# Optimization experiments

Hardware: AMD Instinct MI355X
Metric: run time of the kernel (lower is better)

Reference implementation:

```python
import jax, jax.numpy as jnp
import numpy as np

N, E, DIM, H = 50000, 800000, 64, 4

def setup_inputs() -> dict:
    key = jax.random.key(0)
    k0, k1, k2, k3, k4 = jax.random.split(key, 5)
    h_v = jax.random.normal(k0, (N, DIM), dtype=jnp.float32)
    src = jax.random.randint(k1, (E,), 0, N, dtype=jnp.int64)
    dst = jax.random.randint(k2, (E,), 0, N, dtype=jnp.int64)
    W_fc = jax.random.normal(k3, (DIM * H, DIM), dtype=jnp.float32) * 0.05
    b_fc = jnp.zeros((DIM * H,), dtype=jnp.float32)
    W_pi = jax.random.normal(k4, (1, DIM * H), dtype=jnp.float32) * 0.05
    return {"h_v": h_v, "src": src, "dst": dst, "W_fc": W_fc, "b_fc": b_fc, "W_pi": W_pi}

def reference(h_v, src, dst, W_fc, b_fc, W_pi):
    n, dim = h_v.shape
    heads = W_fc.shape[0] // dim
    # fc: [N, dim] -> [N, H*dim]
    ft = h_v @ W_fc.T + b_fc
    # u_mul_v: per-edge elementwise product of src/dst features  [E, H*dim]
    e = ft[src] * ft[dst]
    # pi + LeakyReLU(0.2): per-edge scalar score  [E]
    s = jax.nn.leaky_relu(e @ W_pi.T, negative_slope=0.2)[:, 0]
    # edge_softmax over incoming edges of each destination node (stable)
    smax = jax.ops.segment_max(s, dst, num_segments=n)
    ex = jnp.exp(s - smax[dst])
    denom = jax.ops.segment_sum(ex, dst, num_segments=n)
    a = ex / denom[dst]                        # [E]
    # u_mul_e + scatter-sum into destination nodes  [N, H*dim]
    agg = jax.ops.segment_sum(ft[src] * a[:, None], dst, num_segments=n)
    # max-pool over heads  [N, dim]
    return agg.reshape(n, heads, dim).max(axis=1)
```

## Files before the change

### kernel.cpp

```cpp
#include <hip/hip_runtime.h>
#include <math.h>

#define DIM 64
#define FDIM 256
#define MAXD 64
#define DEFER_THR 4.0f

typedef _Float16 h2 __attribute__((ext_vector_type(2)));
typedef float f2 __attribute__((ext_vector_type(2)));

__global__ __launch_bounds__(256) void fc_kernel(const float* __restrict__ h,
                                                 const float* __restrict__ W,
                                                 const float* __restrict__ b,
                                                 _Float16* __restrict__ ft,
                                                 int* __restrict__ cnt, int N)
{
    for (int i = blockIdx.x * blockDim.x + threadIdx.x; i < N;
         i += gridDim.x * blockDim.x) cnt[i] = 0;

    int t = threadIdx.x;
    float w[DIM];
#pragma unroll
    for (int j = 0; j < DIM / 4; ++j) {
        float4 v = *(const float4*)(W + (size_t)t * DIM + j * 4);
        w[4 * j + 0] = v.x; w[4 * j + 1] = v.y;
        w[4 * j + 2] = v.z; w[4 * j + 3] = v.w;
    }
    float bt = b[t];
    for (int r = blockIdx.x; r < N; r += gridDim.x) {
        const float4* h4 = (const float4*)(h + (size_t)r * DIM);
        float acc = bt;
#pragma unroll
        for (int j = 0; j < DIM / 4; ++j) {
            float4 hv = h4[j];
            acc = fmaf(hv.x, w[4 * j + 0], acc);
            acc = fmaf(hv.y, w[4 * j + 1], acc);
            acc = fmaf(hv.z, w[4 * j + 2], acc);
            acc = fmaf(hv.w, w[4 * j + 3], acc);
        }
        ft[(size_t)r * FDIM + t] = (_Float16)acc;
    }
}

__global__ void bucket_kernel(const int* __restrict__ src, const int* __restrict__ dst,
                              int* __restrict__ cnt, unsigned short* __restrict__ egrid,
                              int E)
{
    int i = blockIdx.x * blockDim.x + threadIdx.x;
    if (i < E) {
        int d = dst[i];
        int slot = atomicAdd(&cnt[d], 1);
        egrid[(size_t)d * MAXD + slot] = (unsigned short)src[i];
    }
}

__global__ __launch_bounds__(256) void agg_kernel(const _Float16* __restrict__ ft,
                                                  const int* __restrict__ cnt,
                                                  const unsigned short* __restrict__ egrid,
                                                  const float* __restrict__ Wpi,
                                                  float* __restrict__ out, int N)
{
    __shared__ float xb[4][1280];
    int wid = (blockIdx.x * blockDim.x + threadIdx.x) >> 6;
    int wv  = threadIdx.x >> 6;
    int lane = threadIdx.x & 63;
    if (wid >= N) return;
    int q  = lane >> 4;
    int ql = lane & 15;

    h2 fdwh[8];
    {
        const float* wp = Wpi + ql * 16;
        const _Float16* drow = ft + (size_t)wid * FDIM + ql * 16;
        uint4 a = *(const uint4*)(drow);
        uint4 b = *(const uint4*)(drow + 8);
        const h2* da = (const h2*)&a;
        const h2* db = (const h2*)&b;
#pragma unroll
        for (int j = 0; j < 4; ++j) {
            h2 v = da[j], u = db[j];
            fdwh[j].x     = (_Float16)((float)v.x * wp[2 * j + 0]);
            fdwh[j].y     = (_Float16)((float)v.y * wp[2 * j + 1]);
            fdwh[4 + j].x = (_Float16)((float)u.x * wp[8 + 2 * j + 0]);
            fdwh[4 + j].y = (_Float16)((float)u.y * wp[8 + 2 * j + 1]);
        }
    }

    int e0 = wid * MAXD;
    int e1 = e0 + cnt[wid];
    float mq = -INFINITY, lq = 0.f;
    f2 acc2[8];
#pragma unroll
    for (int j = 0; j < 8; ++j) acc2[j] = (f2){0.f, 0.f};

    auto LOAD8 = [&](uint4& a1, uint4& b1, uint4& a2, uint4& b2,
                     bool& v1, bool& v2, int bse) {
        int lo = bse + q, hi = bse + q + 4;
        v1 = lo < e1; v2 = hi < e1;
        int s1 = egrid[v1 ? lo : e0];
        int s2 = egrid[v2 ? hi : e0];
        const _Float16* r1 = ft + (size_t)s1 * FDIM + ql * 16;
        const _Float16* r2 = ft + (size_t)s2 * FDIM + ql * 16;
        a1 = *(const uint4*)(r1);
        b1 = *(const uint4*)(r1 + 8);
        a2 = *(const uint4*)(r2);
        b2 = *(const uint4*)(r2 + 8);
    };
    auto COMP8 = [&](uint4 a1, uint4 b1, uint4 a2, uint4 b2, bool v1, bool v2) {
        const h2* fa1 = (const h2*)&a1; const h2* fb1 = (const h2*)&b1;
        const h2* fa2 = (const h2*)&a2; const h2* fb2 = (const h2*)&b2;
        float p1 = 0.f, p2 = 0.f;
#pragma unroll
        for (int j = 0; j < 4; ++j) {
            p1 = __builtin_amdgcn_fdot2(fa1[j], fdwh[j], p1, false);
            p2 = __builtin_amdgcn_fdot2(fa2[j], fdwh[j], p2, false);
        }
#pragma unroll
        for (int j = 0; j < 4; ++j) {
            p1 = __builtin_amdgcn_fdot2(fb1[j], fdwh[4 + j], p1, false);
            p2 = __builtin_amdgcn_fdot2(fb2[j], fdwh[4 + j], p2, false);
        }
        p1 += __shfl_xor(p1, 1, 64);  p2 += __shfl_xor(p2, 1, 64);
        p1 += __shfl_xor(p1, 2, 64);  p2 += __shfl_xor(p2, 2, 64);
        p1 += __shfl_xor(p1, 4, 64);  p2 += __shfl_xor(p2, 4, 64);
        p1 += __shfl_xor(p1, 8, 64);  p2 += __shfl_xor(p2, 8, 64);
        float s1 = p1 > 0.f ? p1 : 0.2f * p1;
        float s2 = p2 > 0.f ? p2 : 0.2f * p2;
        if (!v1) s1 = -INFINITY;
        if (!v2) s2 = -INFINITY;
        float smax = fmaxf(s1, s2);
        if (smax > mq + DEFER_THR) {
            float sc = __expf(mq - smax);
            lq *= sc;
            f2 sc2 = {sc, sc};
#pragma unroll
            for (int j = 0; j < 8; ++j) acc2[j] *= sc2;
            mq = smax;
        }
        float pe1 = v1 ? __expf(s1 - mq) : 0.f;
        float pe2 = v2 ? __expf(s2 - mq) : 0.f;
        lq += pe1 + pe2;
        f2 pe1v = {pe1, pe1}, pe2v = {pe2, pe2};
#pragma unroll
        for (int j = 0; j < 4; ++j) {
            f2 w1 = {(float)fa1[j].x, (float)fa1[j].y};
            f2 w2 = {(float)fa2[j].x, (float)fa2[j].y};
            acc2[j] = __builtin_elementwise_fma(pe1v, w1,
                       __builtin_elementwise_fma(pe2v, w2, acc2[j]));
            f2 u1 = {(float)fb1[j].x, (float)fb1[j].y};
            f2 u2 = {(float)fb2[j].x, (float)fb2[j].y};
            acc2[4 + j] = __builtin_elementwise_fma(pe1v, u1,
                           __builtin_elementwise_fma(pe2v, u2, acc2[4 + j]));
        }
    };

    if (e0 < e1) {
        uint4 Aa1, Ab1, Aa2, Ab2, Ba1, Bb1, Ba2, Bb2;
        bool Av1, Av2, Bv1, Bv2;
        int base = e0;
        LOAD8(Aa1, Ab1, Aa2, Ab2, Av1, Av2, base);
        while (true) {
            int nxt = base + 8;
            bool more = nxt < e1;
            if (more) LOAD8(Ba1, Bb1, Ba2, Bb2, Bv1, Bv2, nxt);
            COMP8(Aa1, Ab1, Aa2, Ab2, Av1, Av2);
            if (!more) break;
            base = nxt;
            nxt = base + 8;
            more = nxt < e1;
            if (more) LOAD8(Aa1, Ab1, Aa2, Ab2, Av1, Av2, nxt);
            COMP8(Ba1, Bb1, Ba2, Bb2, Bv1, Bv2);
            if (!more) break;
            base = nxt;
        }
    }

    float mstar = fmaxf(mq, __shfl_xor(mq, 16, 64));
    mstar = fmaxf(mstar, __shfl_xor(mstar, 32, 64));
    float sc = (lq > 0.f) ? __expf(mq - mstar) : 0.f;
    float lt = lq * sc;
    lt += __shfl_xor(lt, 16, 64);
    lt += __shfl_xor(lt, 32, 64);
    float inv = (lt > 0.f) ? 1.f / lt : 0.f;

    {
        float* wp = &xb[wv][(unsigned)lane * 20];
        f2 sc2 = {sc, sc};
#pragma unroll
        for (int k = 0; k < 4; ++k) {
            f2 lo = acc2[2 * k] * sc2;
            f2 hi = acc2[2 * k + 1] * sc2;
            *(float4*)(wp + 4 * k) = make_float4(lo.x, lo.y, hi.x, hi.y);
        }
    }
    asm volatile("s_waitcnt lgkmcnt(0)" ::: "memory");
    {
        int col = lane >> 4, jp = lane & 15;
        float A[4];
#pragma unroll
        for (int h = 0; h < 4; ++h) {
            int rowb = (col + 4 * h) * 20 + jp;
            float v0 = xb[wv][rowb];
            float v1 = xb[wv][rowb + 16 * 20];
            float v2 = xb[wv][rowb + 32 * 20];
            float v3 = xb[wv][rowb + 48 * 20];
            A[h] = (v0 + v1) + (v2 + v3);
        }
        float r = fmaxf(fmaxf(A[0], A[1]), fmaxf(A[2], A[3])) * inv;
        out[(size_t)wid * DIM + lane] = r;
    }
}

extern "C" void kernel_launch(void* const* d_in, const int* in_sizes, int n_in,
                              void* d_out, int out_size, void* d_ws, size_t ws_size,
                              hipStream_t stream)
{
    const float* h_v  = (const float*)d_in[0];
    const int*   src  = (const int*)d_in[1];
    const int*   dst  = (const int*)d_in[2];
    const float* W_fc = (const float*)d_in[3];
    const float* b_fc = (const float*)d_in[4];
    const float* W_pi = (const float*)d_in[5];
    float* out = (float*)d_out;

    int N = in_sizes[0] / DIM;
    int E = in_sizes[1];

    _Float16* ft = (_Float16*)d_ws;
    size_t ftB = (((size_t)N * FDIM * 2) + 255) & ~(size_t)255;
    char*  p     = (char*)d_ws + ftB;
    int*   cnt   = (int*)(p);
    unsigned short* egrid = (unsigned short*)(p + 256 * 1024);

    int eb = (E + 255) / 256;
    fc_kernel<<<2048, 256, 0, stream>>>(h_v, W_fc, b_fc, ft, cnt, N);
    bucket_kernel<<<eb, 256, 0, stream>>>(src, dst, cnt, egrid, E);
    int blocks = (N * 64 + 255) / 256;
    agg_kernel<<<blocks, 256, 0, stream>>>(ft, cnt, egrid, W_pi, out, N);
}
```

Measured before the change: 149.1 us.

## Fuse fc and bucketing into one launch, memset counts, pad LDS stride

Merges the fc projection and the edge bucketing kernels into a single launch whose trailing blocks do bucketing, so the two independent stages run concurrently instead of back-to-back. Count zeroing moves to a hipMemsetAsync so bucketing blocks don't race with initialization. The agg kernel's shared-memory transpose buffer stride changes from 20 to 17 floats to cut LDS bank conflicts and shrink shared memory. The risks are an extra memset launch and fc register pressure under launch_bounds(256,2).

```diff
diff --git a/kernel.cpp b/kernel.cpp
--- a/kernel.cpp
+++ b/kernel.cpp
@@ -5,19 +5,27 @@
 #define FDIM 256
 #define MAXD 64
 #define DEFER_THR 4.0f
+#define XSTR 17
 
 typedef _Float16 h2 __attribute__((ext_vector_type(2)));
 typedef float f2 __attribute__((ext_vector_type(2)));
 
-__global__ __launch_bounds__(256) void fc_kernel(const float* __restrict__ h,
-                                                 const float* __restrict__ W,
-                                                 const float* __restrict__ b,
-                                                 _Float16* __restrict__ ft,
-                                                 int* __restrict__ cnt, int N)
+__global__ __launch_bounds__(256, 2) void fc_bucket_kernel(
+        const float* __restrict__ h, const float* __restrict__ W,
+        const float* __restrict__ b, _Float16* __restrict__ ft,
+        const int* __restrict__ src, const int* __restrict__ dst,
+        int* __restrict__ cnt, unsigned short* __restrict__ egrid,
+        int N, int E, int fcB)
 {
-    for (int i = blockIdx.x * blockDim.x + threadIdx.x; i < N;
-         i += gridDim.x * blockDim.x) cnt[i] = 0;
-
+    if (blockIdx.x >= fcB) {
+        int i = (blockIdx.x - fcB) * 256 + threadIdx.x;
+        if (i < E) {
+            int d = dst[i];
+            int slot = atomicAdd(&cnt[d], 1);
+            egrid[(size_t)d * MAXD + slot] = (unsigned short)src[i];
+        }
+        return;
+    }
     int t = threadIdx.x;
     float w[DIM];
 #pragma unroll
@@ -27,7 +35,7 @@
         w[4 * j + 2] = v.z; w[4 * j + 3] = v.w;
     }
     float bt = b[t];
-    for (int r = blockIdx.x; r < N; r += gridDim.x) {
+    for (int r = blockIdx.x; r < N; r += fcB) {
         const float4* h4 = (const float4*)(h + (size_t)r * DIM);
         float acc = bt;
 #pragma unroll
@@ -42,25 +50,13 @@
     }
 }
 
-__global__ void bucket_kernel(const int* __restrict__ src, const int* __restrict__ dst,
-                              int* __restrict__ cnt, unsigned short* __restrict__ egrid,
-                              int E)
-{
-    int i = blockIdx.x * blockDim.x + threadIdx.x;
-    if (i < E) {
-        int d = dst[i];
-        int slot = atomicAdd(&cnt[d], 1);
-        egrid[(size_t)d * MAXD + slot] = (unsigned short)src[i];
-    }
-}
-
 __global__ __launch_bounds__(256) void agg_kernel(const _Float16* __restrict__ ft,
                                                   const int* __restrict__ cnt,
                                                   const unsigned short* __restrict__ egrid,
                                                   const float* __restrict__ Wpi,
                                                   float* __restrict__ out, int N)
 {
-    __shared__ float xb[4][1280];
+    __shared__ float xb[4][64 * XSTR];
     int wid = (blockIdx.x * blockDim.x + threadIdx.x) >> 6;
     int wv  = threadIdx.x >> 6;
     int lane = threadIdx.x & 63;
@@ -184,7 +180,7 @@
     float inv = (lt > 0.f) ? 1.f / lt : 0.f;
 
     {
-        float* wp = &xb[wv][(unsigned)lane * 20];
+        float* wp = &xb[wv][(unsigned)lane * XSTR];
         f2 sc2 = {sc, sc};
 #pragma unroll
         for (int k = 0; k < 4; ++k) {
@@ -199,11 +195,11 @@
         float A[4];
 #pragma unroll
         for (int h = 0; h < 4; ++h) {
-            int rowb = (col + 4 * h) * 20 + jp;
+            int rowb = (col + 4 * h) * XSTR + jp;
             float v0 = xb[wv][rowb];
-            float v1 = xb[wv][rowb + 16 * 20];
-            float v2 = xb[wv][rowb + 32 * 20];
-            float v3 = xb[wv][rowb + 48 * 20];
+            float v1 = xb[wv][rowb + 16 * XSTR];
+            float v2 = xb[wv][rowb + 32 * XSTR];
+            float v3 = xb[wv][rowb + 48 * XSTR];
             A[h] = (v0 + v1) + (v2 + v3);
         }
         float r = fmaxf(fmaxf(A[0], A[1]), fmaxf(A[2], A[3])) * inv;
@@ -232,9 +228,11 @@
     int*   cnt   = (int*)(p);
     unsigned short* egrid = (unsigned short*)(p + 256 * 1024);
 
+    const int fcB = 2048;
     int eb = (E + 255) / 256;
-    fc_kernel<<<2048, 256, 0, stream>>>(h_v, W_fc, b_fc, ft, cnt, N);
-    bucket_kernel<<<eb, 256, 0, stream>>>(src, dst, cnt, egrid, E);
+    hipMemsetAsync(cnt, 0, (size_t)N * sizeof(int), stream);
+    fc_bucket_kernel<<<fcB + eb, 256, 0, stream>>>(h_v, W_fc, b_fc, ft,
+                                                   src, dst, cnt, egrid, N, E, fcB);
     int blocks = (N * 64 + 255) / 256;
     agg_kernel<<<blocks, 256, 0, stream>>>(ft, cnt, egrid, W_pi, out, N);
 }
```

Measured after the change: 204.5 us. +37.2%, slower.
